# Performance work log

Hardware: AMD Instinct MI355X
Metric: run time of the kernel (lower is better)

## Reference

```python
import jax, jax.numpy as jnp
import numpy as np

N_HEAD = 16
N_EMBD = 2048
HEAD_DIM = N_EMBD // N_HEAD  # 128
ROPE_THETA = 10000.0


def _make_rope(T, hd, theta):
    inv = 1.0 / (theta ** (np.arange(0, hd, 2, dtype=np.float32) / hd))  # (hd/2,)
    t = np.arange(T, dtype=np.float32)
    freqs = np.outer(t, inv)  # (T, hd/2)
    return jnp.asarray(np.cos(freqs)), jnp.asarray(np.sin(freqs))


def setup_inputs() -> dict:
    key = jax.random.key(0)
    k1, k2, k3 = jax.random.split(key, 3)
    B, T, C = 2, 2048, N_EMBD
    x = jax.random.normal(k1, (B, T, C), dtype=jnp.float32)
    cos, sin = _make_rope(T, HEAD_DIM, ROPE_THETA)
    w_qkv = jax.random.normal(k2, (3 * C, C), dtype=jnp.float32) * (1.0 / np.sqrt(C))
    w_proj = jax.random.normal(k3, (C, C), dtype=jnp.float32) * (1.0 / np.sqrt(C))
    return {"x": x, "cos": cos, "sin": sin, "w_qkv": w_qkv, "w_proj": w_proj}


def _apply_rope(x, cos, sin):
    # x: (B, H, T, hd); cos/sin: (T, hd/2). Interleaved (even/odd) RoPE.
    B, H, T, hd = x.shape
    xp = x.reshape(B, H, T, hd // 2, 2)
    x1, x2 = xp[..., 0], xp[..., 1]
    c = cos[:T][None, None, :, :]
    s = sin[:T][None, None, :, :]
    even = x1 * c - x2 * s
    odd = x1 * s + x2 * c
    return jnp.stack([even, odd], axis=-1).reshape(B, H, T, hd)


def reference(x, cos, sin, w_qkv, w_proj):
    B, T, C = x.shape
    H, hd = N_HEAD, HEAD_DIM
    qkv = jnp.einsum('btc,dc->btd', x, w_qkv)  # (B,T,3C)
    q, k, v = jnp.split(qkv, 3, axis=-1)
    # (B,T,C) -> (B,H,T,hd)
    q = q.reshape(B, T, H, hd).transpose(0, 2, 1, 3)
    k = k.reshape(B, T, H, hd).transpose(0, 2, 1, 3)
    v = v.reshape(B, T, H, hd).transpose(0, 2, 1, 3)
    q = _apply_rope(q, cos, sin)
    k = _apply_rope(k, cos, sin)
    scale = 1.0 / jnp.sqrt(jnp.asarray(hd, dtype=x.dtype))
    scores = jnp.einsum('bhqd,bhkd->bhqk', q, k) * scale  # (B,H,T,T)
    causal = jnp.tril(jnp.ones((T, T), dtype=bool))
    scores = jnp.where(causal[None, None], scores, jnp.asarray(-jnp.inf, dtype=scores.dtype))
    attn = jax.nn.softmax(scores, axis=-1)
    out = jnp.einsum('bhqk,bhkd->bhqd', attn, v)  # (B,H,T,hd)
    out = out.transpose(0, 2, 1, 3).reshape(B, T, C)
    return jnp.einsum('btc,dc->btd', out, w_proj)
```

## Files before the change

kernel.cpp:

```cpp
#include <hip/hip_runtime.h>
#include <hip/hip_bf16.h>
#include <stdint.h>

typedef __attribute__((ext_vector_type(8))) short bf16x8;
typedef __attribute__((ext_vector_type(4))) float f32x4;

#define B_ 2
#define T_ 2048
#define C_ 2048
#define H_ 16
#define HD_ 128

__device__ inline ushort f2bf(float f) {
  union { float f; uint32_t u; } v; v.f = f;
  uint32_t u = v.u;
  uint32_t r = (u + 0x7fffu + ((u >> 16) & 1u)) >> 16;
  return (ushort)r;
}
__device__ inline float bf2f(ushort h) {
  union { uint32_t u; float f; } v; v.u = ((uint32_t)h) << 16;
  return v.f;
}

typedef const __attribute__((address_space(1))) void* gas1_t;
typedef __attribute__((address_space(3))) void* las3_t;
__device__ inline void gld_lds16(const void* g, void* l) {
  __builtin_amdgcn_global_load_lds((gas1_t)g, (las3_t)l, 16, 0, 0);
}

__global__ __launch_bounds__(256) void k_f2bf(const float* __restrict__ in,
                                              ushort* __restrict__ out, int n4) {
  int i = blockIdx.x * 256 + threadIdx.x;
  if (i < n4) {
    f32x4 v = *(const f32x4*)(in + (size_t)i * 4);
    ushort4 o;
    o.x = f2bf(v[0]); o.y = f2bf(v[1]); o.z = f2bf(v[2]); o.w = f2bf(v[3]);
    *(ushort4*)(out + (size_t)i * 4) = o;
  }
}

template <int OUT_BF16>
__global__ __launch_bounds__(256)
void gemm_bt(const ushort* __restrict__ A, const ushort* __restrict__ Bm,
             void* __restrict__ Cout, int M, int N, int K) {
  __shared__ ushort lA[2][128 * 32];
  __shared__ ushort lB[2][128 * 32];
  const int tid = threadIdx.x;
  const int wid = tid >> 6, lane = tid & 63;
  const int bx = blockIdx.x, by = blockIdx.y;
  const size_t rowA0 = (size_t)by * 128, colB0 = (size_t)bx * 128;
  const int sr = lane >> 2, sc = (lane & 3) * 8;

  const ushort* Abase = A + rowA0 * K + sc;
  const ushort* Bbase = Bm + colB0 * K + sc;

  auto stage = [&](int buf, int kt) {
    const ushort* Ak = Abase + (size_t)kt * 32;
    const ushort* Bk = Bbase + (size_t)kt * 32;
    for (int i = 0; i < 2; i++) {
      int chunk = wid * 2 + i;
      int row = chunk * 16 + sr;
      gld_lds16(Ak + (size_t)row * K, &lA[buf][chunk * 512]);
      gld_lds16(Bk + (size_t)row * K, &lB[buf][chunk * 512]);
    }
  };

  f32x4 acc[4][4];
  const f32x4 zf = {0.f, 0.f, 0.f, 0.f};
  for (int i = 0; i < 4; i++)
    for (int j = 0; j < 4; j++) acc[i][j] = zf;

  const int wr = (wid >> 1) * 64, wc = (wid & 1) * 64;
  const int lr = lane & 15, lk = (lane >> 4) * 8;

  stage(0, 0);
  __syncthreads();
  const int NT = K / 32;
  int buf = 0;
  for (int kt = 0; kt < NT; kt++) {
    if (kt + 1 < NT) stage(buf ^ 1, kt + 1);
    bf16x8 af[4], bfr[4];
    for (int i = 0; i < 4; i++)
      af[i] = *(const bf16x8*)&lA[buf][(wr + i * 16 + lr) * 32 + lk];
    for (int j = 0; j < 4; j++)
      bfr[j] = *(const bf16x8*)&lB[buf][(wc + j * 16 + lr) * 32 + lk];
    for (int i = 0; i < 4; i++)
      for (int j = 0; j < 4; j++)
        acc[i][j] = __builtin_amdgcn_mfma_f32_16x16x32_bf16(af[i], bfr[j],
                                                            acc[i][j], 0, 0, 0);
    __syncthreads();
    buf ^= 1;
  }
  const int lq = (lane >> 4) * 4;
  for (int i = 0; i < 4; i++)
    for (int j = 0; j < 4; j++)
      for (int r = 0; r < 4; r++) {
        size_t row = rowA0 + wr + i * 16 + lq + r;
        size_t col = colB0 + wc + j * 16 + lr;
        float v = acc[i][j][r];
        if (OUT_BF16)
          ((ushort*)Cout)[row * (size_t)N + col] = f2bf(v);
        else
          ((float*)Cout)[row * (size_t)N + col] = v;
      }
}

__global__ __launch_bounds__(256)
void rope_split(const ushort* __restrict__ qkv, const float* __restrict__ cosb,
                const float* __restrict__ sinb, ushort* __restrict__ Qr,
                ushort* __restrict__ Kr, ushort* __restrict__ Vr) {
  const int bt = blockIdx.x;
  const int b = bt >> 11, t = bt & 2047;
  const ushort* base = qkv + (size_t)bt * (3 * C_);
  const int tid = threadIdx.x;
  const float rs = 0.08838834764831845f;
  for (int i = 0; i < 4; i++) {
    int idx = tid + i * 256;
    int h = idx >> 6, p = idx & 63;
    float c = cosb[t * 64 + p], s = sinb[t * 64 + p];
    size_t src = (size_t)h * HD_ + 2 * p;
    size_t dst = (((size_t)(b * H_ + h)) * T_ + t) * HD_ + 2 * p;
    float x1 = bf2f(base[src]), x2 = bf2f(base[src + 1]);
    Qr[dst] = f2bf((x1 * c - x2 * s) * rs);
    Qr[dst + 1] = f2bf((x1 * s + x2 * c) * rs);
    x1 = bf2f(base[C_ + src]); x2 = bf2f(base[C_ + src + 1]);
    Kr[dst] = f2bf(x1 * c - x2 * s);
    Kr[dst + 1] = f2bf(x1 * s + x2 * c);
    Vr[dst] = base[2 * C_ + src];
    Vr[dst + 1] = base[2 * C_ + src + 1];
  }
}

__global__ __launch_bounds__(256)
void attn_fwd(const ushort* __restrict__ Qr, const ushort* __restrict__ Kr,
              const ushort* __restrict__ Vr, ushort* __restrict__ Out) {
  __shared__ ushort lK[32][136];
  __shared__ ushort lV[128][40];
  __shared__ ushort lP[4][16][40];
  const int tid = threadIdx.x, wid = tid >> 6, lane = tid & 63;
  const int bh = blockIdx.y;
  const int b = bh >> 4, h = bh & 15;
  const int pr = blockIdx.x;
  const int lr = lane & 15, g = lane >> 4, lk8 = g * 8;
  const f32x4 zf = {0.f, 0.f, 0.f, 0.f};

  const ushort* Kp = Kr + (size_t)bh * T_ * HD_;
  const ushort* Vp = Vr + (size_t)bh * T_ * HD_;

  int rK[2], cK[2], rV[2], cV[2];
  for (int i = 0; i < 2; i++) {
    int chunk = tid + i * 256;
    rK[i] = chunk >> 4; cK[i] = (chunk & 15) * 8;
    rV[i] = chunk & 31; cV[i] = (chunk >> 5) * 8;
  }

  for (int seg = 0; seg < 2; ++seg) {
    const int qt = seg ? (31 - pr) : pr;
    const int qbase = qt * 64 + wid * 16;
    const ushort* Qp = Qr + ((size_t)bh * T_ + qbase) * HD_;

    bf16x8 qf[4];
    for (int dc = 0; dc < 4; dc++)
      qf[dc] = *(const bf16x8*)(Qp + (size_t)lr * HD_ + dc * 32 + lk8);

    f32x4 o[8];
    for (int dt = 0; dt < 8; dt++) o[dt] = zf;
    float m = -1e30f, l = 0.f;

    bf16x8 kreg[2], vreg[2];
    auto load_tile = [&](int kt) {
      for (int i = 0; i < 2; i++) {
        kreg[i] = *(const bf16x8*)(Kp + ((size_t)(kt * 32 + rK[i])) * HD_ + cK[i]);
        vreg[i] = *(const bf16x8*)(Vp + ((size_t)(kt * 32 + rV[i])) * HD_ + cV[i]);
      }
    };

    const int nkt = 2 * qt + 2;
    load_tile(0);
    for (int kt = 0; kt < nkt; kt++) {
      __syncthreads();
      for (int i = 0; i < 2; i++) {
        *(bf16x8*)&lK[rK[i]][cK[i]] = kreg[i];
        for (int j = 0; j < 8; j++) lV[cV[i] + j][rV[i]] = (ushort)vreg[i][j];
      }
      if (kt + 1 < nkt) load_tile(kt + 1);
      __syncthreads();
      if (kt * 32 <= qbase + 15) {
        f32x4 s[2];
        for (int kn = 0; kn < 2; kn++) {
          f32x4 a = zf;
          for (int dc = 0; dc < 4; dc++) {
            bf16x8 kf = *(const bf16x8*)&lK[kn * 16 + lr][dc * 32 + lk8];
            a = __builtin_amdgcn_mfma_f32_16x16x32_bf16(kf, qf[dc], a, 0, 0, 0);
          }
          s[kn] = a;
        }
        const int qg = qbase + lr;
        if (kt * 32 + 31 > qbase) {
          for (int kn = 0; kn < 2; kn++) {
            int k0 = kt * 32 + kn * 16 + g * 4;
            for (int r = 0; r < 4; r++)
              if (k0 + r > qg) s[kn][r] = -1e30f;
          }
        }
        float pm = fmaxf(fmaxf(fmaxf(s[0][0], s[0][1]), fmaxf(s[0][2], s[0][3])),
                         fmaxf(fmaxf(s[1][0], s[1][1]), fmaxf(s[1][2], s[1][3])));
        pm = fmaxf(pm, __shfl_xor(pm, 16, 64));
        pm = fmaxf(pm, __shfl_xor(pm, 32, 64));
        if (!__all(pm - m <= 5.0f)) {
          float mn = fmaxf(m, pm);
          float a = __expf(m - mn);
          for (int dt = 0; dt < 8; dt++)
            for (int r = 0; r < 4; r++) o[dt][r] *= a;
          l *= a;
          m = mn;
        }
        float p[8];
        float rsum = 0.f;
        for (int kn = 0; kn < 2; kn++)
          for (int r = 0; r < 4; r++) {
            float pv = __expf(s[kn][r] - m);
            p[kn * 4 + r] = pv;
            rsum += pv;
          }
        rsum += __shfl_xor(rsum, 16, 64);
        rsum += __shfl_xor(rsum, 32, 64);
        l += rsum;
        for (int kn = 0; kn < 2; kn++) {
          ushort2 w0, w1;
          w0.x = f2bf(p[kn * 4 + 0]); w0.y = f2bf(p[kn * 4 + 1]);
          w1.x = f2bf(p[kn * 4 + 2]); w1.y = f2bf(p[kn * 4 + 3]);
          *(ushort2*)&lP[wid][lr][kn * 16 + g * 4] = w0;
          *(ushort2*)&lP[wid][lr][kn * 16 + g * 4 + 2] = w1;
        }
        bf16x8 pf = *(const bf16x8*)&lP[wid][lr][lk8];
        for (int dt = 0; dt < 8; dt++) {
          bf16x8 vf = *(const bf16x8*)&lV[dt * 16 + lr][lk8];
          o[dt] = __builtin_amdgcn_mfma_f32_16x16x32_bf16(vf, pf, o[dt], 0, 0, 0);
        }
      }
    }
    float inv = 1.0f / l;
    int qg = qbase + lr;
    size_t obase = ((size_t)b * T_ + qg) * C_ + (size_t)h * HD_;
    for (int dt = 0; dt < 8; dt++) {
      ushort4 w;
      w.x = f2bf(o[dt][0] * inv);
      w.y = f2bf(o[dt][1] * inv);
      w.z = f2bf(o[dt][2] * inv);
      w.w = f2bf(o[dt][3] * inv);
      *(ushort4*)&Out[obase + dt * 16 + g * 4] = w;
    }
  }
}

extern "C" void kernel_launch(void* const* d_in, const int* in_sizes, int n_in,
                              void* d_out, int out_size, void* d_ws,
                              size_t ws_size, hipStream_t stream) {
  (void)in_sizes; (void)n_in; (void)out_size; (void)ws_size;
  const float* x = (const float*)d_in[0];
  const float* cosb = (const float*)d_in[1];
  const float* sinb = (const float*)d_in[2];
  const float* w_qkv = (const float*)d_in[3];
  const float* w_proj = (const float*)d_in[4];

  char* ws = (char*)d_ws;
  ushort* wqkvb = (ushort*)(ws);
  ushort* wprojb = (ushort*)(ws + 25165824);
  ushort* xb = (ushort*)(ws + 25165824 + 8388608);
  ushort* qkv = (ushort*)(ws + 25165824 + 8388608 + 16777216);
  ushort* kr = (ushort*)(ws + 25165824 + 8388608 + 16777216 + 50331648);
  ushort* vr = (ushort*)(ws + 25165824 + 8388608 + 16777216 + 50331648 + 16777216);
  ushort* qr = xb;
  ushort* attn_out = qkv;

  k_f2bf<<<8192, 256, 0, stream>>>(x, xb, 2097152);
  k_f2bf<<<12288, 256, 0, stream>>>(w_qkv, wqkvb, 3145728);
  k_f2bf<<<4096, 256, 0, stream>>>(w_proj, wprojb, 1048576);

  gemm_bt<1><<<dim3(48, 32), 256, 0, stream>>>(xb, wqkvb, (void*)qkv,
                                               4096, 6144, 2048);
  rope_split<<<4096, 256, 0, stream>>>(qkv, cosb, sinb, qr, kr, vr);
  attn_fwd<<<dim3(16, 32), 256, 0, stream>>>(qr, kr, vr, attn_out);
  gemm_bt<0><<<dim3(16, 32), 256, 0, stream>>>(attn_out, wprojb, d_out,
                                               4096, 2048, 2048);
}
```

Measured before the change: 410.8 us.

## Replace QKV GEMM with 256x256-tile, 8-wave pipelined kernel using swizzled LDS

Adds a new QKV projection GEMM that uses 256x256 output tiles with 512 threads and a double-buffered LDS layout with an XOR swizzle. It staggers the A and B tile loads across two barrier phases, raises wave priority around the MFMA blocks, and remaps block IDs across 8 groups for better L2 locality. The aim is more reuse per LDS byte and more overlap of global loads with MFMA work than the old 128x128 kernel gave. The cost is heavy register pressure from 128 accumulator floats per thread and hand-placed waitcnt and barrier logic that could be fragile. The output-projection GEMM is de-templated to fp32 output only.

```diff
diff --git a/kernel.cpp b/kernel.cpp
--- a/kernel.cpp
+++ b/kernel.cpp
@@ -10,6 +10,8 @@
 #define C_ 2048
 #define H_ 16
 #define HD_ 128
+
+#define MFENCE asm volatile("" ::: "memory")
 
 __device__ inline ushort f2bf(float f) {
   union { float f; uint32_t u; } v; v.f = f;
@@ -39,10 +41,128 @@
   }
 }
 
-template <int OUT_BF16>
+__global__ __launch_bounds__(512, 2)
+void gemm256(const ushort* __restrict__ A, const ushort* __restrict__ Bm,
+             ushort* __restrict__ Cout, int M, int N, int K) {
+  __shared__ ushort lds[2][16384];
+  const int tid = threadIdx.x;
+  const int wid = tid >> 6, lane = tid & 63;
+  const int wm = wid >> 2, wn = wid & 3;
+
+  const int nwg = gridDim.x;
+  const int cpx = nwg >> 3;
+  const int bid = blockIdx.x;
+  const int wg = (bid & 7) * cpx + (bid >> 3);
+  const int ntx = N >> 8;
+  const int bm = wg / ntx, bn = wg % ntx;
+  const size_t trow0 = (size_t)bm * 256, tcol0 = (size_t)bn * 256;
+
+  const size_t Kb = (size_t)K * 2;
+  {
+  }
+  const int s = tid * 16;
+  const int rp = s >> 7;
+  const int sub = (s & 127) ^ ((rp & 7) << 4);
+  const int r_st = rp * 2 + (sub >> 6);
+  const int kb_st = sub & 63;
+  const char* aSrc = (const char*)A + (trow0 + r_st) * Kb + kb_st;
+  const char* bSrc = (const char*)Bm + (tcol0 + r_st) * Kb + kb_st;
+
+  auto stA = [&](int bf, int h, int kt) {
+    gld_lds16(aSrc + (size_t)h * 128 * Kb + (size_t)kt * 64,
+              &lds[bf][h * 4096 + wid * 512]);
+  };
+  auto stB = [&](int bf, int h, int kt) {
+    gld_lds16(bSrc + (size_t)h * 128 * Kb + (size_t)kt * 64,
+              &lds[bf][8192 + h * 4096 + wid * 512]);
+  };
+
+  int aOff[8], bOff[4];
+  {
+    const int li = lane & 15, cb = (lane >> 4) * 16;
+#pragma unroll
+    for (int mf = 0; mf < 8; ++mf) {
+      int rl = mf * 32 + wm * 16 + li;
+      int h = rl >> 7, r = rl & 127;
+      int byte = (((r >> 1) * 128) + ((r & 1) * 64) + cb) ^ (((r >> 1) & 7) << 4);
+      aOff[mf] = h * 4096 + (byte >> 1);
+    }
+#pragma unroll
+    for (int nf = 0; nf < 4; ++nf) {
+      int cl = nf * 64 + wn * 16 + li;
+      int h = cl >> 7, c = cl & 127;
+      int byte = (((c >> 1) * 128) + ((c & 1) * 64) + cb) ^ (((c >> 1) & 7) << 4);
+      bOff[nf] = 8192 + h * 4096 + (byte >> 1);
+    }
+  }
+
+  f32x4 acc[8][4];
+  const f32x4 zf = {0.f, 0.f, 0.f, 0.f};
+#pragma unroll
+  for (int i = 0; i < 8; ++i)
+#pragma unroll
+    for (int j = 0; j < 4; ++j) acc[i][j] = zf;
+
+  stB(0, 0, 0); stB(0, 1, 0); stA(0, 0, 0); stA(0, 1, 0);
+  stB(1, 0, 1); stB(1, 1, 1);
+  asm volatile("s_waitcnt vmcnt(2)" ::: "memory");
+  __builtin_amdgcn_s_barrier();
+  MFENCE;
+
+  const int NT = K >> 5;
+  bf16x8 bfr[4], af[4];
+  for (int k = 0; k < NT; ++k) {
+    const int bf = k & 1, bn2 = bf ^ 1;
+    const int ka = (k + 1 < NT) ? k + 1 : NT - 1;
+    const int kb2 = (k + 2 < NT) ? k + 2 : NT - 1;
+#pragma unroll
+    for (int nf = 0; nf < 4; ++nf) bfr[nf] = *(const bf16x8*)&lds[bf][bOff[nf]];
+#pragma unroll
+    for (int i = 0; i < 4; ++i) af[i] = *(const bf16x8*)&lds[bf][aOff[i]];
+    stA(bn2, 0, ka); stA(bn2, 1, ka);
+    MFENCE; __builtin_amdgcn_s_barrier(); MFENCE;
+    __builtin_amdgcn_s_setprio(1);
+#pragma unroll
+    for (int mf = 0; mf < 4; ++mf)
+#pragma unroll
+      for (int nf = 0; nf < 4; ++nf)
+        acc[mf][nf] = __builtin_amdgcn_mfma_f32_16x16x32_bf16(af[mf], bfr[nf],
+                                                              acc[mf][nf], 0, 0, 0);
+    __builtin_amdgcn_s_setprio(0);
+    MFENCE; __builtin_amdgcn_s_barrier(); MFENCE;
+#pragma unroll
+    for (int i = 0; i < 4; ++i) af[i] = *(const bf16x8*)&lds[bf][aOff[4 + i]];
+    stB(bf, 0, kb2); stB(bf, 1, kb2);
+    MFENCE; __builtin_amdgcn_s_barrier(); MFENCE;
+    __builtin_amdgcn_s_setprio(1);
+#pragma unroll
+    for (int mf = 0; mf < 4; ++mf)
+#pragma unroll
+      for (int nf = 0; nf < 4; ++nf)
+        acc[4 + mf][nf] = __builtin_amdgcn_mfma_f32_16x16x32_bf16(af[mf], bfr[nf],
+                                                                  acc[4 + mf][nf], 0, 0, 0);
+    __builtin_amdgcn_s_setprio(0);
+    asm volatile("s_waitcnt vmcnt(2)" ::: "memory");
+    MFENCE; __builtin_amdgcn_s_barrier(); MFENCE;
+  }
+
+  const int orow = (lane >> 4) * 4, ocol = lane & 15;
+#pragma unroll
+  for (int mf = 0; mf < 8; ++mf) {
+    const size_t row0 = trow0 + mf * 32 + wm * 16 + orow;
+#pragma unroll
+    for (int nf = 0; nf < 4; ++nf) {
+      const size_t col = tcol0 + nf * 64 + wn * 16 + ocol;
+#pragma unroll
+      for (int r = 0; r < 4; ++r)
+        Cout[(row0 + r) * (size_t)N + col] = f2bf(acc[mf][nf][r]);
+    }
+  }
+}
+
 __global__ __launch_bounds__(256)
 void gemm_bt(const ushort* __restrict__ A, const ushort* __restrict__ Bm,
-             void* __restrict__ Cout, int M, int N, int K) {
+             float* __restrict__ Cout, int M, int N, int K) {
   __shared__ ushort lA[2][128 * 32];
   __shared__ ushort lB[2][128 * 32];
   const int tid = threadIdx.x;
@@ -97,11 +217,7 @@
       for (int r = 0; r < 4; r++) {
         size_t row = rowA0 + wr + i * 16 + lq + r;
         size_t col = colB0 + wc + j * 16 + lr;
-        float v = acc[i][j][r];
-        if (OUT_BF16)
-          ((ushort*)Cout)[row * (size_t)N + col] = f2bf(v);
-        else
-          ((float*)Cout)[row * (size_t)N + col] = v;
+        Cout[row * (size_t)N + col] = acc[i][j][r];
       }
 }
 
@@ -278,10 +394,9 @@
   k_f2bf<<<12288, 256, 0, stream>>>(w_qkv, wqkvb, 3145728);
   k_f2bf<<<4096, 256, 0, stream>>>(w_proj, wprojb, 1048576);
 
-  gemm_bt<1><<<dim3(48, 32), 256, 0, stream>>>(xb, wqkvb, (void*)qkv,
-                                               4096, 6144, 2048);
+  gemm256<<<384, 512, 0, stream>>>(xb, wqkvb, qkv, 4096, 6144, 2048);
   rope_split<<<4096, 256, 0, stream>>>(qkv, cosb, sinb, qr, kr, vr);
   attn_fwd<<<dim3(16, 32), 256, 0, stream>>>(qr, kr, vr, attn_out);
-  gemm_bt<0><<<dim3(16, 32), 256, 0, stream>>>(attn_out, wprojb, d_out,
-                                               4096, 2048, 2048);
-}
+  gemm_bt<<<dim3(16, 32), 256, 0, stream>>>(attn_out, wprojb, (float*)d_out,
+                                            4096, 2048, 2048);
+}
```

Result: no change. 410.7 us (-0.0%).
